# Optimization experiments

Measured on AMD Instinct MI355X. Metric: run time of the kernel, lower is better.

Reference implementation:

```python
import jax, jax.numpy as jnp
import numpy as np
from jax import lax

SCORE_THRESHOLD = 0.02
IOU_THRESHOLD = 0.5
NUM_CLASSES = 80
MAX_DETECTIONS = 10  # tf.image.non_max_suppression max_output_size in the source
ANCHORS = np.array([[1.08, 1.19], [3.42, 4.41], [6.63, 11.38], [9.42, 5.11], [16.62, 10.52]], dtype=np.float32)


def setup_inputs() -> dict:
    key = jax.random.key(0)
    k1, _ = jax.random.split(key)
    B, H, W = 16, 76, 76
    A = ANCHORS.shape[0]
    feats = jax.random.normal(k1, (B, H, W, A * (5 + NUM_CLASSES)), dtype=jnp.float32)
    anchors = jnp.asarray(ANCHORS)
    return {"feats": feats, "anchors": anchors}


def yolo_head(feats, anchors, num_classes):
    """Standard YOLOv2 decode (interpret_prediction)."""
    B, H, W, _ = feats.shape
    A = anchors.shape[0]
    feats = feats.reshape(B, H, W, A, 5 + num_classes)
    gy, gx = jnp.meshgrid(jnp.arange(H), jnp.arange(W), indexing="ij")
    grid = jnp.stack([gx, gy], axis=-1).astype(feats.dtype)  # [H,W,2] in (x,y) order
    conv_dims = jnp.array([W, H], dtype=feats.dtype)
    box_xy = (jax.nn.sigmoid(feats[..., 0:2]) + grid[None, :, :, None, :]) / conv_dims
    box_wh = jnp.exp(feats[..., 2:4]) * anchors[None, None, None, :, :] / conv_dims
    box_confidence = jax.nn.sigmoid(feats[..., 4:5])
    box_class_probs = jax.nn.softmax(feats[..., 5:], axis=-1)
    return box_xy, box_wh, box_confidence, box_class_probs


def _postprocess(feats, anchors):
    box_xy, box_wh, box_confidence, box_class_probs = yolo_head(feats, anchors, NUM_CLASSES)
    box_mins = box_xy - box_wh / 2.0
    box_maxes = box_xy + box_wh / 2.0
    # [y_min, x_min, y_max, x_max] as in the source (indices 1 then 0)
    boxes = jnp.concatenate([box_mins[..., 1:2], box_mins[..., 0:1], box_maxes[..., 1:2], box_maxes[..., 0:1]], axis=-1)
    box_scores = box_confidence * box_class_probs           # [B,H,W,A,C]
    box_classes = jnp.argmax(box_scores, axis=-1)           # [B,H,W,A]
    box_class_scores = jnp.max(box_scores, axis=-1)         # [B,H,W,A]

    # tf.boolean_mask flattens across all dims; emulate with fixed shapes by
    # marking below-threshold candidates as invalid (score -1).
    flat_boxes = boxes.reshape(-1, 4)                       # [N,4]
    flat_scores = box_class_scores.reshape(-1)              # [N]
    flat_classes = box_classes.reshape(-1)                  # [N]
    scores_work = jnp.where(flat_scores >= SCORE_THRESHOLD, flat_scores, -1.0)

    N = flat_boxes.shape[0]
    areas = jnp.maximum(flat_boxes[:, 2] - flat_boxes[:, 0], 0.0) * jnp.maximum(flat_boxes[:, 3] - flat_boxes[:, 1], 0.0)
    idx_range = jnp.arange(N)

    def step(sw, _):
        idx = jnp.argmax(sw)
        s = sw[idx]
        valid = s >= SCORE_THRESHOLD
        box = flat_boxes[idx]                               # [4] = y1,x1,y2,x2
        iy1 = jnp.maximum(box[0], flat_boxes[:, 0])
        ix1 = jnp.maximum(box[1], flat_boxes[:, 1])
        iy2 = jnp.minimum(box[2], flat_boxes[:, 2])
        ix2 = jnp.minimum(box[3], flat_boxes[:, 3])
        inter = jnp.maximum(iy2 - iy1, 0.0) * jnp.maximum(ix2 - ix1, 0.0)
        box_area = jnp.maximum(box[2] - box[0], 0.0) * jnp.maximum(box[3] - box[1], 0.0)
        iou = inter / (box_area + areas - inter + 1e-9)
        suppress = (iou > IOU_THRESHOLD) | (idx_range == idx)
        sw_new = jnp.where(valid & suppress, -1.0, sw)
        row = jnp.concatenate([box, s[None], flat_classes[idx].astype(jnp.float32)[None]])  # [6]
        row = jnp.where(valid, row, jnp.zeros_like(row))
        return sw_new, row

    _, rows = lax.scan(step, scores_work, None, length=MAX_DETECTIONS)
    return rows  # [MAX_DETECTIONS, 6] = [y1,x1,y2,x2,score,class]; zero rows are padding


def reference(feats, anchors):
    return _postprocess(feats, anchors)
```

## Files before the change

### kernel.cpp

```cpp
#include <hip/hip_runtime.h>
#include <stdint.h>

#define N_CAND 462080
#define NBINS  2048
#define HPAD   16
#define HIST_BLOCKS 32
#define COMPACT_BLOCKS 64
#define TARGET 256u
#define SMAX   1024
#define SCORE_THR 0.02f
#define DEC_BLOCKS 1805
#define C_CNT 0
#define C_BIN 16
#define C_HD  32
#define C_CD  48


__global__ __launch_bounds__(256) void decode_kernel(
    const float* __restrict__ feats,
    float* __restrict__ scores, unsigned char* __restrict__ cls,
    unsigned int* __restrict__ ctrl, unsigned int* __restrict__ hist)
{
    const int t = threadIdx.x;
    const int ci = blockIdx.x * 256 + t;

    if (blockIdx.x == 0) {
        if (t == 0) { ctrl[C_HD] = 0u; ctrl[C_CD] = 0u; }
        for (int i = t; i < NBINS; i += 256) hist[i * HPAD] = 0u;
    }

    const float4* __restrict__ p = reinterpret_cast<const float4*>(feats + (size_t)ci * 85);
    float4 r[21];
#pragma unroll
    for (int i = 0; i < 21; ++i) r[i] = p[i];
    const float f84 = (feats + (size_t)ci * 85)[84];

    float m = r[1].y; int cb = 0;
    if (r[1].z > m) { m = r[1].z; cb = 1; }
    if (r[1].w > m) { m = r[1].w; cb = 2; }
#pragma unroll
    for (int i = 2; i < 21; ++i) {
        const int b = i * 4 - 5;
        if (r[i].x > m) { m = r[i].x; cb = b; }
        if (r[i].y > m) { m = r[i].y; cb = b + 1; }
        if (r[i].z > m) { m = r[i].z; cb = b + 2; }
        if (r[i].w > m) { m = r[i].w; cb = b + 3; }
    }
    if (f84 > m) { m = f84; cb = 79; }

    float s0 = __expf(r[1].y - m);
    float s1 = __expf(r[1].z - m);
    float s2 = __expf(r[1].w - m);
    float s3 = 0.f;
#pragma unroll
    for (int i = 2; i < 21; ++i) {
        s0 += __expf(r[i].x - m);
        s1 += __expf(r[i].y - m);
        s2 += __expf(r[i].z - m);
        s3 += __expf(r[i].w - m);
    }
    s3 += __expf(f84 - m);
    const float ssum = (s0 + s1) + (s2 + s3);

    const float conf = 1.0f / (1.0f + __expf(-r[1].x));
    const float score = conf / ssum;
    scores[ci] = (score >= SCORE_THR) ? score : -1.0f;
    cls[ci] = (unsigned char)cb;
}

__global__ __launch_bounds__(1024) void hist_cutoff_kernel(
    const float* __restrict__ scores, unsigned int* __restrict__ hist,
    unsigned int* __restrict__ ctrl)
{
    __shared__ unsigned int lh[NBINS];
    __shared__ unsigned int pa[1024], pb[1024];
    __shared__ int lastf;
    const int t = threadIdx.x;

    lh[2 * t] = 0u; lh[2 * t + 1] = 0u;
    __syncthreads();

    for (int i = blockIdx.x * 1024 + t; i < N_CAND; i += HIST_BLOCKS * 1024) {
        float s = scores[i];
        if (s >= SCORE_THR) {
            int bin = (int)(s * (float)NBINS);
            bin = bin > (NBINS - 1) ? (NBINS - 1) : bin;
            atomicAdd(&lh[bin], 1u);
        }
    }
    __syncthreads();
    unsigned v0 = lh[2 * t], v1 = lh[2 * t + 1];
    if (v0) atomicAdd(&hist[(2 * t) * HPAD], v0);
    if (v1) atomicAdd(&hist[(2 * t + 1) * HPAD], v1);
    __syncthreads();

    if (t == 0) {
        __threadfence();
        unsigned old = atomicAdd(&ctrl[C_HD], 1u);
        lastf = (old == HIST_BLOCKS - 1) ? 1 : 0;
    }
    __syncthreads();
    if (!lastf) return;
    if (t == 0) __threadfence();
    __syncthreads();

    unsigned b0 = hist[(2 * t) * HPAD];
    unsigned b1 = hist[(2 * t + 1) * HPAD];
    lh[2 * t] = b0; lh[2 * t + 1] = b1;
    pa[t] = b0 + b1;
    __syncthreads();

    unsigned int* srcb = pa; unsigned int* dstb = pb;
    for (int off = 1; off < 1024; off <<= 1) {
        unsigned v = srcb[t] + ((t + off < 1024) ? srcb[t + off] : 0u);
        dstb[t] = v;
        __syncthreads();
        unsigned int* tmp = srcb; srcb = dstb; dstb = tmp;
    }
    unsigned St = srcb[t];
    unsigned Sn = (t < 1023) ? srcb[t + 1] : 0u;

    if (t == 0) {
        ctrl[C_CNT] = 0u;
        if (St < TARGET) ctrl[C_BIN] = 0u;
    }
    if (St >= TARGET && Sn < TARGET) {
        unsigned run = Sn + lh[2 * t + 1];
        ctrl[C_BIN] = (run >= TARGET) ? (unsigned)(2 * t + 1) : (unsigned)(2 * t);
    }
}

__device__ inline float4 decode_box(const float* __restrict__ feats,
                                    const float* __restrict__ anchors, int ci)
{
    int a = ci % 5;
    int cell = ci / 5;
    int gx = cell % 76;
    int gy = (cell / 76) % 76;
    const float* f = feats + (long long)ci * 85;
    float bx = (1.0f / (1.0f + __expf(-f[0])) + (float)gx) / 76.0f;
    float by = (1.0f / (1.0f + __expf(-f[1])) + (float)gy) / 76.0f;
    float bw = __expf(f[2]) * anchors[2 * a]     / 76.0f;
    float bh = __expf(f[3]) * anchors[2 * a + 1] / 76.0f;
    return make_float4(by - bh * 0.5f, bx - bw * 0.5f,
                       by + bh * 0.5f, bx + bw * 0.5f);
}

__global__ __launch_bounds__(1024) void compact_nms_kernel(
    const float* __restrict__ scores, unsigned int* __restrict__ ctrl,
    float* __restrict__ lscore, int* __restrict__ lidx,
    const float* __restrict__ feats, const float* __restrict__ anchors,
    const unsigned char* __restrict__ cls, float* __restrict__ out)
{
    __shared__ unsigned long long wkey[16];
    __shared__ unsigned long long bkey;
    __shared__ float4 bbox;
    __shared__ int lastf;
    const int t = threadIdx.x;

    const int cut = (int)ctrl[C_BIN];
    for (int i = blockIdx.x * 1024 + t; i < N_CAND; i += COMPACT_BLOCKS * 1024) {
        float sw = scores[i];
        if (sw >= SCORE_THR) {
            int bin = (int)(sw * (float)NBINS);
            bin = bin > (NBINS - 1) ? (NBINS - 1) : bin;
            if (bin >= cut) {
                unsigned pos = atomicAdd(&ctrl[C_CNT], 1u);
                if (pos < SMAX) { lscore[pos] = sw; lidx[pos] = i; }
            }
        }
    }
    __syncthreads();
    if (t == 0) {
        __threadfence();
        unsigned old = atomicAdd(&ctrl[C_CD], 1u);
        lastf = (old == COMPACT_BLOCKS - 1) ? 1 : 0;
    }
    __syncthreads();
    if (!lastf) return;
    if (t == 0) __threadfence();
    __syncthreads();

    unsigned cnt = ctrl[C_CNT];
    int n = (cnt < (unsigned)SMAX) ? (int)cnt : SMAX;

    unsigned long long key = 0ull;
    float4 mb = make_float4(0.f, 0.f, 0.f, 0.f);
    float  msc = 0.f, mcls = 0.f;
    unsigned midx = 0xFFFFFFFFu;
    bool aliveb = false;
    if (t < n) {
        msc  = lscore[t];
        midx = (unsigned)lidx[t];
        key  = ((unsigned long long)__float_as_uint(msc) << 32)
             | (unsigned long long)(0xFFFFFFFFu - midx);
        mb   = decode_box(feats, anchors, (int)midx);
        mcls = (float)cls[midx];
        aliveb = true;
    }

    for (int r = 0; r < 10; ++r) {
        unsigned long long k0 = aliveb ? key : 0ull;
#pragma unroll
        for (int msk = 32; msk > 0; msk >>= 1) {
            unsigned long long o = __shfl_xor(k0, msk);
            k0 = (o > k0) ? o : k0;
        }
        if ((t & 63) == 0) wkey[t >> 6] = k0;
        __syncthreads();
        if (t < 16) {
            unsigned long long v = wkey[t];
#pragma unroll
            for (int msk = 8; msk > 0; msk >>= 1) {
                unsigned long long o = __shfl_xor(v, msk);
                v = (o > v) ? o : v;
            }
            if (t == 0) bkey = v;
        }
        __syncthreads();

        unsigned long long wk = bkey;
        bool have = (wk != 0ull);
        unsigned widx = have ? (0xFFFFFFFFu - (unsigned)(wk & 0xFFFFFFFFull)) : 0xFFFFFFFFu;

        if (have && aliveb && midx == widx) {
            bbox = mb;
            out[r * 6 + 0] = mb.x;
            out[r * 6 + 1] = mb.y;
            out[r * 6 + 2] = mb.z;
            out[r * 6 + 3] = mb.w;
            out[r * 6 + 4] = msc;
            out[r * 6 + 5] = mcls;
            aliveb = false;
        }
        if (!have && t == 0) {
#pragma unroll
            for (int q = 0; q < 6; ++q) out[r * 6 + q] = 0.f;
        }
        __syncthreads();

        if (have && aliveb) {
            float4 ab = bbox;
            float aarea = fmaxf(ab.z - ab.x, 0.f) * fmaxf(ab.w - ab.y, 0.f);
            float iy1 = fmaxf(ab.x, mb.x);
            float ix1 = fmaxf(ab.y, mb.y);
            float iy2 = fminf(ab.z, mb.z);
            float ix2 = fminf(ab.w, mb.w);
            float inter = fmaxf(iy2 - iy1, 0.f) * fmaxf(ix2 - ix1, 0.f);
            float carea = fmaxf(mb.z - mb.x, 0.f) * fmaxf(mb.w - mb.y, 0.f);
            float iou = inter / (aarea + carea - inter + 1e-9f);
            if (iou > 0.5f) aliveb = false;
        }
    }
}

extern "C" void kernel_launch(void* const* d_in, const int* in_sizes, int n_in,
                              void* d_out, int out_size, void* d_ws, size_t ws_size,
                              hipStream_t stream) {
    const float* feats   = (const float*)d_in[0];
    const float* anchors = (const float*)d_in[1];
    char* ws = (char*)d_ws;

    unsigned int*   ctrl   = (unsigned int*)(ws + 0);
    unsigned int*   hist   = (unsigned int*)(ws + 256);
    float*          lscore = (float*)(ws + 131328);
    int*            lidx   = (int*)(ws + 135424);
    float*          scores = (float*)(ws + 139520);
    unsigned char*  cls    = (unsigned char*)(ws + 1987840);
    float*          out    = (float*)d_out;

    decode_kernel      <<<DEC_BLOCKS, 256, 0, stream>>>(feats, scores, cls, ctrl, hist);
    hist_cutoff_kernel <<<HIST_BLOCKS, 1024, 0, stream>>>(scores, hist, ctrl);
    compact_nms_kernel <<<COMPACT_BLOCKS, 1024, 0, stream>>>(scores, ctrl, lscore, lidx,
                                                             feats, anchors, cls, out);
}
```

Measured before the change: 59.81 us.

## Swizzle decode blocks per XCD, skip unused box floats, widen histogram grid

Remaps decode block indices so that each of the 8 XCDs handles a contiguous range of candidates, aiming for better L2 locality on the chiplet layout. It also stops loading the first float4 (the box coordinates, which this kernel never uses), which cuts the bytes each thread reads. The histogram kernel grid grows from 32 to 96 blocks to raise parallelism. The swizzle depends on round-robin block-to-XCD dispatch, and the hand-coded 226/225 split must add up to exactly 1805 blocks.

After: 57.42 us, median of 3. 1.04x faster.

```diff
diff --git a/kernel.cpp b/kernel.cpp
--- a/kernel.cpp
+++ b/kernel.cpp
@@ -4,7 +4,7 @@
 #define N_CAND 462080
 #define NBINS  2048
 #define HPAD   16
-#define HIST_BLOCKS 32
+#define HIST_BLOCKS 96
 #define COMPACT_BLOCKS 64
 #define TARGET 256u
 #define SMAX   1024
@@ -22,47 +22,51 @@
     unsigned int* __restrict__ ctrl, unsigned int* __restrict__ hist)
 {
     const int t = threadIdx.x;
-    const int ci = blockIdx.x * 256 + t;
-
-    if (blockIdx.x == 0) {
+    const int bid = blockIdx.x;
+    const int xcd = bid & 7, bix = bid >> 3;
+    const int swz = (xcd < 5 ? xcd * 226 : 1130 + (xcd - 5) * 225) + bix;
+    const int ci = swz * 256 + t;
+
+    if (bid == 0) {
         if (t == 0) { ctrl[C_HD] = 0u; ctrl[C_CD] = 0u; }
         for (int i = t; i < NBINS; i += 256) hist[i * HPAD] = 0u;
     }
 
-    const float4* __restrict__ p = reinterpret_cast<const float4*>(feats + (size_t)ci * 85);
-    float4 r[21];
-#pragma unroll
-    for (int i = 0; i < 21; ++i) r[i] = p[i];
-    const float f84 = (feats + (size_t)ci * 85)[84];
-
-    float m = r[1].y; int cb = 0;
-    if (r[1].z > m) { m = r[1].z; cb = 1; }
-    if (r[1].w > m) { m = r[1].w; cb = 2; }
-#pragma unroll
-    for (int i = 2; i < 21; ++i) {
-        const int b = i * 4 - 5;
-        if (r[i].x > m) { m = r[i].x; cb = b; }
-        if (r[i].y > m) { m = r[i].y; cb = b + 1; }
-        if (r[i].z > m) { m = r[i].z; cb = b + 2; }
-        if (r[i].w > m) { m = r[i].w; cb = b + 3; }
+    const float* __restrict__ fr = feats + (size_t)ci * 85;
+    const float4* __restrict__ p = reinterpret_cast<const float4*>(fr + 4);
+    float4 q[20];
+#pragma unroll
+    for (int i = 0; i < 20; ++i) q[i] = p[i];
+    const float f84 = fr[84];
+
+    float m = q[0].y; int cb = 0;
+    if (q[0].z > m) { m = q[0].z; cb = 1; }
+    if (q[0].w > m) { m = q[0].w; cb = 2; }
+#pragma unroll
+    for (int i = 1; i < 20; ++i) {
+        const int b = i * 4 - 1;
+        if (q[i].x > m) { m = q[i].x; cb = b; }
+        if (q[i].y > m) { m = q[i].y; cb = b + 1; }
+        if (q[i].z > m) { m = q[i].z; cb = b + 2; }
+        if (q[i].w > m) { m = q[i].w; cb = b + 3; }
     }
     if (f84 > m) { m = f84; cb = 79; }
 
-    float s0 = __expf(r[1].y - m);
-    float s1 = __expf(r[1].z - m);
-    float s2 = __expf(r[1].w - m);
+    float s0 = __expf(q[0].y - m);
+    float s1 = __expf(q[0].z - m);
+    float s2 = __expf(q[0].w - m);
     float s3 = 0.f;
 #pragma unroll
-    for (int i = 2; i < 21; ++i) {
-        s0 += __expf(r[i].x - m);
-        s1 += __expf(r[i].y - m);
-        s2 += __expf(r[i].z - m);
-        s3 += __expf(r[i].w - m);
+    for (int i = 1; i < 20; ++i) {
+        s0 += __expf(q[i].x - m);
+        s1 += __expf(q[i].y - m);
+        s2 += __expf(q[i].z - m);
+        s3 += __expf(q[i].w - m);
     }
     s3 += __expf(f84 - m);
     const float ssum = (s0 + s1) + (s2 + s3);
 
-    const float conf = 1.0f / (1.0f + __expf(-r[1].x));
+    const float conf = 1.0f / (1.0f + __expf(-q[0].x));
     const float score = conf / ssum;
     scores[ci] = (score >= SCORE_THR) ? score : -1.0f;
     cls[ci] = (unsigned char)cb;
```
